# Optimization experiments

Hardware: AMD Instinct MI355X
Metric: run time of the kernel (lower is better)

## Reference

```python
import jax, jax.numpy as jnp
import numpy as np

B, C, H, W = 16, 1024, 64, 64
CH = C // 2
LN_EPS = 1e-5  # F.layer_norm default eps

def setup_inputs() -> dict:
    key = jax.random.key(0)
    ks = jax.random.split(key, 5)
    x = jax.random.normal(ks[0], (B, C, H, W), dtype=jnp.float32)
    # 1x1 conv weights, shape (out_ch, in_ch)
    w_qr = jax.random.normal(ks[1], (1, C), dtype=jnp.float32) * 0.02
    w_vr = jax.random.normal(ks[2], (CH, C), dtype=jnp.float32) * 0.02
    w_ql = jax.random.normal(ks[3], (CH, C), dtype=jnp.float32) * 0.02
    w_vl = jax.random.normal(ks[4], (CH, C), dtype=jnp.float32) * 0.02
    return {"x": x, "w_qr": w_qr, "w_vr": w_vr, "w_ql": w_ql, "w_vl": w_vl}

def reference(x, w_qr, w_vr, w_ql, w_vl):
    b, c, h, w = x.shape
    ch, hw = c // 2, h * w
    # mmcv ConvModule: 1x1 conv (no bias, no norm) + default ReLU activation
    conv = lambda wt: jax.nn.relu(jnp.einsum('bchw,oc->bohw', x, wt))

    # --- spatial attention branch ---
    input_x = conv(w_vr).reshape(b, ch, hw)                       # (b, ch, hw)
    mask = jax.nn.softmax(conv(w_qr).reshape(b, hw), axis=1)      # (b, hw)
    context = jnp.einsum('bcn,bn->bc', input_x, mask)             # (b, ch)
    # layer_norm over (ch,1,1) -> normalize over channel dim, no affine
    mu = jnp.mean(context, axis=1, keepdims=True)
    var = jnp.mean((context - mu) ** 2, axis=1, keepdims=True)
    spatial_attn = jax.nn.sigmoid((context - mu) * jax.lax.rsqrt(var + LN_EPS))[:, :, None]  # (b, ch, 1)

    # --- channel attention branch ---
    g_x = conv(w_ql)                                              # (b, ch, h, w)
    avg_x = jax.nn.softmax(jnp.mean(g_x, axis=(2, 3)), axis=1)    # (b, ch)
    theta_x = conv(w_vl).reshape(b, ch, hw)                       # (b, ch, hw)
    channel_attn = jax.nn.sigmoid(jnp.einsum('bc,bcn->bn', avg_x, theta_x))[:, None, :]  # (b, 1, hw)

    # --- combine ---
    sequence = (spatial_attn * channel_attn).reshape(b, ch, h, w)  # outer product (b, ch, hw)
    parallel = (channel_attn + spatial_attn).reshape(b, ch, h, w)  # broadcast sum
    sk_attn = jnp.concatenate([sequence, parallel], axis=1)        # (b, c, h, w)
    return x * sk_attn + x
```

## Files before the change

### kernel.cpp

```cpp
#include <hip/hip_runtime.h>
#include <cstdint>
#include <cstddef>

#define BATCH 16
#define CIN   1024
#define CH    512
#define HW    4096

static constexpr float LN_EPS = 1e-5f;

typedef __bf16 bf16x8 __attribute__((ext_vector_type(8)));
typedef float  f32x4  __attribute__((ext_vector_type(4)));

__device__ __forceinline__ float sigmoidf_(float v) { return 1.0f / (1.0f + __expf(-v)); }

__device__ __forceinline__ unsigned short f2bf(float f) {
    union { float f; uint32_t u; } c; c.f = f;
    uint32_t r = (c.u + 0x7fffu + ((c.u >> 16) & 1u)) >> 16;
    return (unsigned short)r;
}

#define GLOAD_LDS16(g, l)                                                  \
    __builtin_amdgcn_global_load_lds(                                      \
        (const __attribute__((address_space(1))) void*)(g),                \
        (__attribute__((address_space(3))) void*)(l), 16, 0, 0)

__global__ __launch_bounds__(256) void prep_k(
    const float* __restrict__ x, const float* __restrict__ wqr,
    const float* __restrict__ wvr, const float* __restrict__ wql,
    const float* __restrict__ wvl,
    unsigned short* __restrict__ xt, float* __restrict__ maskpre,
    unsigned short* __restrict__ wA, unsigned short* __restrict__ wB)
{
    __shared__ float t[64][65];
    const int tid = threadIdx.x;
    if (blockIdx.x >= 16384) {
        const int j = (blockIdx.x - 16384) * 256 + tid;
        if (j < 1024 * 1024) {
            const int row = j >> 10, col = j & 1023;
            const float v = (row < 512) ? wql[row * 1024 + col]
                                        : wvr[(row - 512) * 1024 + col];
            wA[j] = f2bf(v);
        } else {
            const int k = j - 1024 * 1024;
            wB[k] = f2bf(wvl[k]);
        }
        return;
    }
    const int nb = blockIdx.x & 63;
    const int cb = (blockIdx.x >> 6) & 15;
    const int b  = blockIdx.x >> 10;
    const int c0 = cb * 64;
    const int n0 = nb * 64;
    const int tx = tid & 15, ty = tid >> 4;
    const float* xb = x + ((size_t)b * CIN + c0) * HW + n0;
#pragma unroll
    for (int rr = 0; rr < 4; ++rr) {
        const int row = ty + rr * 16;
        float4 v = *(const float4*)(xb + (size_t)row * HW + tx * 4);
        t[row][tx * 4 + 0] = v.x; t[row][tx * 4 + 1] = v.y;
        t[row][tx * 4 + 2] = v.z; t[row][tx * 4 + 3] = v.w;
    }
    __syncthreads();
    const int n  = tid >> 2;
    const int cp = (tid & 3) * 16;
    __align__(16) unsigned short tmp[16];
    float part = 0.f;
#pragma unroll
    for (int i = 0; i < 16; ++i) {
        const float v = t[cp + i][n];
        tmp[i] = f2bf(v);
        part = fmaf(wqr[c0 + cp + i], v, part);
    }
    unsigned short* dst = xt + ((size_t)b * HW + n0 + n) * CIN + c0 + cp;
    ((uint4*)dst)[0] = ((const uint4*)tmp)[0];
    ((uint4*)dst)[1] = ((const uint4*)tmp)[1];
    part += __shfl_xor(part, 1);
    part += __shfl_xor(part, 2);
    if ((tid & 3) == 0) atomicAdd(&maskpre[(size_t)b * HW + n0 + n], part);
}

__global__ __launch_bounds__(512) void mfma_gemm256(
    const unsigned short* __restrict__ xt,
    const unsigned short* __restrict__ wst,
    const int MT, const int phase,
    const float* __restrict__ maskp,
    const float* __restrict__ avgx,
    float* __restrict__ gmean,
    float* __restrict__ ctx,
    float* __restrict__ cattnp)
{
    const int nwg = gridDim.x;
    const int per = nwg >> 3;
    const int bid = blockIdx.x;
    const int nid = (bid & 7) * per + (bid >> 3);
    const int mt = nid % MT;
    const int r2 = nid / MT;
    const int nb = r2 & 15;
    const int b  = r2 >> 4;
    const int o0 = mt * 256;
    const int n0 = nb * 256;

    const int tid  = threadIdx.x;
    const int w    = tid >> 6;
    const int lane = tid & 63;
    const int wm = w >> 2;
    const int wn = w & 3;
    const int lr = lane & 15;
    const int hi = lane >> 4;
    const int lr7 = lane & 7;

    __shared__ __align__(16) unsigned short lds[2 * 2 * 2 * 8192];

    f32x4 acc[8][4];
#pragma unroll
    for (int mi = 0; mi < 8; ++mi)
#pragma unroll
        for (int nj = 0; nj < 4; ++nj) acc[mi][nj] = (f32x4){0.f, 0.f, 0.f, 0.f};

    const int sr  = lane >> 3;
    const int ssl = (lane & 7) ^ sr;
    const unsigned short* gA[2][2];
    const unsigned short* gB[2][2];
#pragma unroll
    for (int h = 0; h < 2; ++h)
#pragma unroll
        for (int j = 0; j < 2; ++j) {
            const int row = (w * 2 + j) * 8 + sr;
            gA[h][j] = wst + (size_t)(o0 + h * 128 + row) * CIN + ssl * 8;
            gB[h][j] = xt + ((size_t)b * HW + n0 + h * 128 + row) * CIN + ssl * 8;
        }

#define STG(m, h, tt) do {                                                  \
        unsigned short* lb_ = lds + ((((tt) & 1) * 4) + (m) * 2 + (h)) * 8192 \
                              + (w * 2) * 512;                              \
        const unsigned short* s0_ = ((m) ? gB[h][0] : gA[h][0]) + (tt) * 64; \
        const unsigned short* s1_ = ((m) ? gB[h][1] : gA[h][1]) + (tt) * 64; \
        GLOAD_LDS16(s0_, lb_);                                              \
        GLOAD_LDS16(s1_, lb_ + 512);                                        \
    } while (0)

    const int aoff = lr * 64;
    const int boff = (wn & 1) * 4096 + lr * 64;
    const int sl0 = ((0 + hi) ^ lr7) * 8;
    const int sl1 = ((4 + hi) ^ lr7) * 8;

    bf16x8 bf[4][2];

#define PHASE_BODY(q, c, STAGE_STMT, GATE_STMT) do {                        \
        const unsigned short* Ab_ = lds + ((c) * 4 + wm) * 8192;            \
        const unsigned short* Bb_ = lds + ((c) * 4 + 2 + (wn >> 1)) * 8192; \
        if ((q) == 0) {                                                     \
            _Pragma("unroll")                                               \
            for (int nj = 0; nj < 4; ++nj) {                                \
                bf[nj][0] = *(const bf16x8*)(Bb_ + boff + nj * 1024 + sl0); \
                bf[nj][1] = *(const bf16x8*)(Bb_ + boff + nj * 1024 + sl1); \
            }                                                               \
        }                                                                   \
        bf16x8 af_[2][2];                                                   \
        _Pragma("unroll")                                                   \
        for (int mi = 0; mi < 2; ++mi) {                                    \
            af_[mi][0] = *(const bf16x8*)(Ab_ + ((q) * 32 + mi * 16) * 64 + aoff + sl0); \
            af_[mi][1] = *(const bf16x8*)(Ab_ + ((q) * 32 + mi * 16) * 64 + aoff + sl1); \
        }                                                                   \
        STAGE_STMT;                                                         \
        GATE_STMT;                                                          \
        asm volatile("s_barrier" ::: "memory");                             \
        __builtin_amdgcn_s_setprio(1);                                      \
        _Pragma("unroll")                                                   \
        for (int mi = 0; mi < 2; ++mi)                                      \
            _Pragma("unroll")                                               \
            for (int nj = 0; nj < 4; ++nj) {                                \
                acc[(q) * 2 + mi][nj] = __builtin_amdgcn_mfma_f32_16x16x32_bf16( \
                    af_[mi][0], bf[nj][0], acc[(q) * 2 + mi][nj], 0, 0, 0); \
                acc[(q) * 2 + mi][nj] = __builtin_amdgcn_mfma_f32_16x16x32_bf16( \
                    af_[mi][1], bf[nj][1], acc[(q) * 2 + mi][nj], 0, 0, 0); \
            }                                                               \
        __builtin_amdgcn_s_setprio(0);                                      \
        __builtin_amdgcn_sched_barrier(0);                                  \
        asm volatile("s_barrier" ::: "memory");                             \
    } while (0)

    STG(0, 0, 0); STG(0, 1, 0); STG(1, 0, 0); STG(1, 1, 0);
    STG(1, 0, 1); STG(1, 1, 1); STG(0, 0, 1);
    asm volatile("s_waitcnt vmcnt(6)" ::: "memory");
    asm volatile("s_barrier" ::: "memory");

#pragma unroll 2
    for (int kt = 0; kt < 16; ++kt) {
        const int c = kt & 1;
        PHASE_BODY(0, c, { if (kt < 15) STG(0, 1, kt + 1); }, {});
        PHASE_BODY(1, c, { if (kt < 14) STG(1, 0, kt + 2); }, {});
        PHASE_BODY(2, c, { if (kt < 14) STG(1, 1, kt + 2); }, {});
        PHASE_BODY(3, c, { if (kt < 14) STG(0, 0, kt + 2); },
                   { if (kt < 14)       asm volatile("s_waitcnt vmcnt(6)" ::: "memory");
                     else if (kt == 14) asm volatile("s_waitcnt vmcnt(0)" ::: "memory"); });
    }
#undef PHASE_BODY
#undef STG

    const int quad = hi;
    if (phase == 0) {
        if (mt < 2) {
#pragma unroll
            for (int mr = 0; mr < 8; ++mr)
#pragma unroll
                for (int r = 0; r < 4; ++r) {
                    float v = 0.f;
#pragma unroll
                    for (int nj = 0; nj < 4; ++nj) v += fmaxf(acc[mr][nj][r], 0.f);
                    v += __shfl_xor(v, 1); v += __shfl_xor(v, 2);
                    v += __shfl_xor(v, 4); v += __shfl_xor(v, 8);
                    if (lr == 0)
                        atomicAdd(&gmean[b * CH + o0 + wm * 128 + mr * 16 + quad * 4 + r], v);
                }
        } else {
            float ew[4];
#pragma unroll
            for (int nj = 0; nj < 4; ++nj)
                ew[nj] = __expf(fmaxf(maskp[(size_t)b * HW + n0 + wn * 64 + nj * 16 + lr], 0.f));
#pragma unroll
            for (int mr = 0; mr < 8; ++mr)
#pragma unroll
                for (int r = 0; r < 4; ++r) {
                    float v = 0.f;
#pragma unroll
                    for (int nj = 0; nj < 4; ++nj)
                        v += fmaxf(acc[mr][nj][r], 0.f) * ew[nj];
                    v += __shfl_xor(v, 1); v += __shfl_xor(v, 2);
                    v += __shfl_xor(v, 4); v += __shfl_xor(v, 8);
                    if (lr == 0)
                        atomicAdd(&ctx[b * CH + (o0 - 512) + wm * 128 + mr * 16 + quad * 4 + r], v);
                }
        }
    } else {
        float colsum[4] = {0.f, 0.f, 0.f, 0.f};
#pragma unroll
        for (int mr = 0; mr < 8; ++mr) {
            float aw[4];
#pragma unroll
            for (int r = 0; r < 4; ++r)
                aw[r] = avgx[b * CH + o0 + wm * 128 + mr * 16 + quad * 4 + r];
#pragma unroll
            for (int nj = 0; nj < 4; ++nj)
#pragma unroll
                for (int r = 0; r < 4; ++r)
                    colsum[nj] += fmaxf(acc[mr][nj][r], 0.f) * aw[r];
        }
#pragma unroll
        for (int nj = 0; nj < 4; ++nj) {
            float v = colsum[nj];
            v += __shfl_xor(v, 16);
            v += __shfl_xor(v, 32);
            if (lane < 16)
                atomicAdd(&cattnp[(size_t)b * HW + n0 + wn * 64 + nj * 16 + lane], v);
        }
    }
}

__global__ __launch_bounds__(256) void smch_S_k(const float* __restrict__ gmean,
                                                const float* __restrict__ maskp,
                                                float* __restrict__ avgx,
                                                float* __restrict__ sden)
{
    __shared__ float red[256];
    const int tid = threadIdx.x;
    if (blockIdx.x < 16) {
        const int b = blockIdx.x;
        const float* src = gmean + b * CH;
        float* dst = avgx + b * CH;
        const float v0 = src[tid]       * (1.f / HW);
        const float v1 = src[tid + 256] * (1.f / HW);
        red[tid] = fmaxf(v0, v1); __syncthreads();
        for (int s = 128; s > 0; s >>= 1) { if (tid < s) red[tid] = fmaxf(red[tid], red[tid + s]); __syncthreads(); }
        const float mx = red[0]; __syncthreads();
        const float e0 = __expf(v0 - mx), e1 = __expf(v1 - mx);
        red[tid] = e0 + e1; __syncthreads();
        for (int s = 128; s > 0; s >>= 1) { if (tid < s) red[tid] += red[tid + s]; __syncthreads(); }
        const float inv = 1.f / red[0];
        dst[tid] = e0 * inv; dst[tid + 256] = e1 * inv;
    } else {
        const int b = blockIdx.x - 16;
        const float* row = maskp + (size_t)b * HW;
        float s = 0.f;
        for (int i = tid; i < HW; i += 256) s += __expf(fmaxf(row[i], 0.f));
        red[tid] = s; __syncthreads();
        for (int st = 128; st > 0; st >>= 1) { if (tid < st) red[tid] += red[tid + st]; __syncthreads(); }
        if (tid == 0) sden[b] = red[0];
    }
}

__global__ __launch_bounds__(256) void lnsig_k(const float* __restrict__ ctx,
                                               const float* __restrict__ sden,
                                               float* __restrict__ sattn,
                                               float* __restrict__ cattnp)
{
    const int tid = threadIdx.x;
    if (blockIdx.x >= 16) {
        const int i = (blockIdx.x - 16) * 256 + tid;
        cattnp[i] = sigmoidf_(cattnp[i]);
        return;
    }
    const int b = blockIdx.x;
    const float invS = 1.f / sden[b];
    const float* src = ctx + b * CH;
    __shared__ float red[256];
    const float v0 = src[tid] * invS, v1 = src[tid + 256] * invS;
    red[tid] = v0 + v1; __syncthreads();
    for (int s = 128; s > 0; s >>= 1) { if (tid < s) red[tid] += red[tid + s]; __syncthreads(); }
    const float mu = red[0] * (1.f / CH); __syncthreads();
    const float d0 = v0 - mu, d1 = v1 - mu;
    red[tid] = d0 * d0 + d1 * d1; __syncthreads();
    for (int s = 128; s > 0; s >>= 1) { if (tid < s) red[tid] += red[tid + s]; __syncthreads(); }
    const float rs = rsqrtf(red[0] * (1.f / CH) + LN_EPS);
    sattn[b * CH + tid]       = sigmoidf_(d0 * rs);
    sattn[b * CH + tid + 256] = sigmoidf_(d1 * rs);
}

__global__ __launch_bounds__(256) void final_k(const float* __restrict__ x,
                                               const float* __restrict__ sattn,
                                               const float* __restrict__ cattnp,
                                               float* __restrict__ out)
{
    const int c = blockIdx.x;
    const int b = blockIdx.y;
    const float s = sattn[b * CH + (c & (CH - 1))];
    const bool seq = c < CH;
    const float4* xr = (const float4*)(x + ((size_t)b * CIN + c) * HW);
    const float4* cr = (const float4*)(cattnp + (size_t)b * HW);
    float4* orow = (float4*)(out + ((size_t)b * CIN + c) * HW);
    for (int i = threadIdx.x; i < HW / 4; i += 256) {
        const float4 xv = xr[i], cv = cr[i];
        float4 f;
        if (seq) { f.x = s * cv.x; f.y = s * cv.y; f.z = s * cv.z; f.w = s * cv.w; }
        else     { f.x = s + cv.x; f.y = s + cv.y; f.z = s + cv.z; f.w = s + cv.w; }
        float4 o;
        o.x = fmaf(xv.x, f.x, xv.x);
        o.y = fmaf(xv.y, f.y, xv.y);
        o.z = fmaf(xv.z, f.z, xv.z);
        o.w = fmaf(xv.w, f.w, xv.w);
        orow[i] = o;
    }
}

extern "C" void kernel_launch(void* const* d_in, const int* in_sizes, int n_in,
                              void* d_out, int out_size, void* d_ws, size_t ws_size,
                              hipStream_t stream)
{
    const float* x    = (const float*)d_in[0];
    const float* w_qr = (const float*)d_in[1];
    const float* w_vr = (const float*)d_in[2];
    const float* w_ql = (const float*)d_in[3];
    const float* w_vl = (const float*)d_in[4];
    float* out = (float*)d_out;

    unsigned short* xt = (unsigned short*)d_out;
    unsigned short* wA = xt + (size_t)BATCH * HW * CIN;
    unsigned short* wB = wA + 1024 * CIN;

    float* ws     = (float*)d_ws;
    float* maskp  = ws;
    float* gmean  = maskp + BATCH * HW;
    float* ctx    = gmean + BATCH * CH;
    float* cattnp = ctx   + BATCH * CH;
    float* avgx   = cattnp + BATCH * HW;
    float* sattn  = avgx  + BATCH * CH;
    float* sden   = sattn + BATCH * CH;

    hipMemsetAsync(maskp, 0,
                   (size_t)(BATCH * HW * 2 + BATCH * CH * 2) * sizeof(float), stream);

    prep_k<<<22528, 256, 0, stream>>>(x, w_qr, w_vr, w_ql, w_vl, xt, maskp, wA, wB);

    mfma_gemm256<<<1024, 512, 0, stream>>>(
        xt, wA, 4, 0, maskp, nullptr, gmean, ctx, nullptr);
    smch_S_k<<<32, 256, 0, stream>>>(gmean, maskp, avgx, sden);
    mfma_gemm256<<<512, 512, 0, stream>>>(
        xt, wB, 2, 1, nullptr, avgx, nullptr, nullptr, cattnp);
    lnsig_k<<<272, 256, 0, stream>>>(ctx, sden, sattn, cattnp);
    final_k<<<dim3(CIN, BATCH), 256, 0, stream>>>(x, sattn, cattnp, out);
}
```

Baseline: 721.4 us.

## Make GEMM blocks loop over all M tiles with a continuous K pipeline

Each GEMM workgroup now owns one (batch, 256-column N tile) and walks every 256-row M tile in sequence. The load pipeline runs unbroken across M-tile boundaries, and the per-tile epilogue reductions run inside the loop before the accumulators are reset. This drops the grid to 256 blocks, removing pipeline prologue and drain per tile and letting the B tile stay hot in L2 across M tiles. In exchange there is less parallelism: 256 blocks of 512 threads on a 256-CU part is one wave per CU. Epilogue work inside the loop may also stall the prefetch pipeline.

```diff
diff --git a/kernel.cpp b/kernel.cpp
--- a/kernel.cpp
+++ b/kernel.cpp
@@ -90,15 +90,9 @@
     float* __restrict__ ctx,
     float* __restrict__ cattnp)
 {
-    const int nwg = gridDim.x;
-    const int per = nwg >> 3;
     const int bid = blockIdx.x;
-    const int nid = (bid & 7) * per + (bid >> 3);
-    const int mt = nid % MT;
-    const int r2 = nid / MT;
-    const int nb = r2 & 15;
-    const int b  = r2 >> 4;
-    const int o0 = mt * 256;
+    const int nb = bid & 15;
+    const int b  = bid >> 4;
     const int n0 = nb * 256;
 
     const int tid  = threadIdx.x;
@@ -127,15 +121,18 @@
 #pragma unroll
         for (int j = 0; j < 2; ++j) {
             const int row = (w * 2 + j) * 8 + sr;
-            gA[h][j] = wst + (size_t)(o0 + h * 128 + row) * CIN + ssl * 8;
+            gA[h][j] = wst + (size_t)(h * 128 + row) * CIN + ssl * 8;
             gB[h][j] = xt + ((size_t)b * HW + n0 + h * 128 + row) * CIN + ssl * 8;
         }
 
-#define STG(m, h, tt) do {                                                  \
-        unsigned short* lb_ = lds + ((((tt) & 1) * 4) + (m) * 2 + (h)) * 8192 \
+#define STG(m, h, st) do {                                                  \
+        const int ti_ = (st) >> 4, k_ = (st) & 15;                          \
+        unsigned short* lb_ = lds + ((((st) & 1) * 4) + (m) * 2 + (h)) * 8192 \
                               + (w * 2) * 512;                              \
-        const unsigned short* s0_ = ((m) ? gB[h][0] : gA[h][0]) + (tt) * 64; \
-        const unsigned short* s1_ = ((m) ? gB[h][1] : gA[h][1]) + (tt) * 64; \
+        const unsigned short* s0_ = (m) ? (gB[h][0] + k_ * 64)              \
+                                        : (gA[h][0] + ti_ * (256 * CIN) + k_ * 64); \
+        const unsigned short* s1_ = (m) ? (gB[h][1] + k_ * 64)              \
+                                        : (gA[h][1] + ti_ * (256 * CIN) + k_ * 64); \
         GLOAD_LDS16(s0_, lb_);                                              \
         GLOAD_LDS16(s1_, lb_ + 512);                                        \
     } while (0)
@@ -181,81 +178,90 @@
         asm volatile("s_barrier" ::: "memory");                             \
     } while (0)
 
+    const int T = MT * 16;
+
     STG(0, 0, 0); STG(0, 1, 0); STG(1, 0, 0); STG(1, 1, 0);
     STG(1, 0, 1); STG(1, 1, 1); STG(0, 0, 1);
     asm volatile("s_waitcnt vmcnt(6)" ::: "memory");
     asm volatile("s_barrier" ::: "memory");
 
+    const int quad = hi;
 #pragma unroll 2
-    for (int kt = 0; kt < 16; ++kt) {
-        const int c = kt & 1;
-        PHASE_BODY(0, c, { if (kt < 15) STG(0, 1, kt + 1); }, {});
-        PHASE_BODY(1, c, { if (kt < 14) STG(1, 0, kt + 2); }, {});
-        PHASE_BODY(2, c, { if (kt < 14) STG(1, 1, kt + 2); }, {});
-        PHASE_BODY(3, c, { if (kt < 14) STG(0, 0, kt + 2); },
-                   { if (kt < 14)       asm volatile("s_waitcnt vmcnt(6)" ::: "memory");
-                     else if (kt == 14) asm volatile("s_waitcnt vmcnt(0)" ::: "memory"); });
+    for (int step = 0; step < T; ++step) {
+        const int c = step & 1;
+        PHASE_BODY(0, c, { if (step + 1 < T) STG(0, 1, step + 1); }, {});
+        PHASE_BODY(1, c, { if (step + 2 < T) STG(1, 0, step + 2); }, {});
+        PHASE_BODY(2, c, { if (step + 2 < T) STG(1, 1, step + 2); }, {});
+        PHASE_BODY(3, c, { if (step + 2 < T) STG(0, 0, step + 2); },
+                   { if (step + 2 < T)       asm volatile("s_waitcnt vmcnt(6)" ::: "memory");
+                     else if (step + 2 == T) asm volatile("s_waitcnt vmcnt(0)" ::: "memory"); });
+
+        if ((step & 15) == 15) {
+            const int ti = step >> 4;
+            if (phase == 0) {
+                if (ti < 2) {
+#pragma unroll
+                    for (int mr = 0; mr < 8; ++mr)
+#pragma unroll
+                        for (int r = 0; r < 4; ++r) {
+                            float v = 0.f;
+#pragma unroll
+                            for (int nj = 0; nj < 4; ++nj) v += fmaxf(acc[mr][nj][r], 0.f);
+                            v += __shfl_xor(v, 1); v += __shfl_xor(v, 2);
+                            v += __shfl_xor(v, 4); v += __shfl_xor(v, 8);
+                            if (lr == 0)
+                                atomicAdd(&gmean[b * CH + ti * 256 + wm * 128 + mr * 16 + quad * 4 + r], v);
+                        }
+                } else {
+                    float ew[4];
+#pragma unroll
+                    for (int nj = 0; nj < 4; ++nj)
+                        ew[nj] = __expf(fmaxf(maskp[(size_t)b * HW + n0 + wn * 64 + nj * 16 + lr], 0.f));
+#pragma unroll
+                    for (int mr = 0; mr < 8; ++mr)
+#pragma unroll
+                        for (int r = 0; r < 4; ++r) {
+                            float v = 0.f;
+#pragma unroll
+                            for (int nj = 0; nj < 4; ++nj)
+                                v += fmaxf(acc[mr][nj][r], 0.f) * ew[nj];
+                            v += __shfl_xor(v, 1); v += __shfl_xor(v, 2);
+                            v += __shfl_xor(v, 4); v += __shfl_xor(v, 8);
+                            if (lr == 0)
+                                atomicAdd(&ctx[b * CH + (ti - 2) * 256 + wm * 128 + mr * 16 + quad * 4 + r], v);
+                        }
+                }
+            } else {
+                float colsum[4] = {0.f, 0.f, 0.f, 0.f};
+#pragma unroll
+                for (int mr = 0; mr < 8; ++mr) {
+                    float aw[4];
+#pragma unroll
+                    for (int r = 0; r < 4; ++r)
+                        aw[r] = avgx[b * CH + ti * 256 + wm * 128 + mr * 16 + quad * 4 + r];
+#pragma unroll
+                    for (int nj = 0; nj < 4; ++nj)
+#pragma unroll
+                        for (int r = 0; r < 4; ++r)
+                            colsum[nj] += fmaxf(acc[mr][nj][r], 0.f) * aw[r];
+                }
+#pragma unroll
+                for (int nj = 0; nj < 4; ++nj) {
+                    float v = colsum[nj];
+                    v += __shfl_xor(v, 16);
+                    v += __shfl_xor(v, 32);
+                    if (lane < 16)
+                        atomicAdd(&cattnp[(size_t)b * HW + n0 + wn * 64 + nj * 16 + lane], v);
+                }
+            }
+#pragma unroll
+            for (int mi = 0; mi < 8; ++mi)
+#pragma unroll
+                for (int nj = 0; nj < 4; ++nj) acc[mi][nj] = (f32x4){0.f, 0.f, 0.f, 0.f};
+        }
     }
 #undef PHASE_BODY
 #undef STG
-
-    const int quad = hi;
-    if (phase == 0) {
-        if (mt < 2) {
-#pragma unroll
-            for (int mr = 0; mr < 8; ++mr)
-#pragma unroll
-                for (int r = 0; r < 4; ++r) {
-                    float v = 0.f;
-#pragma unroll
-                    for (int nj = 0; nj < 4; ++nj) v += fmaxf(acc[mr][nj][r], 0.f);
-                    v += __shfl_xor(v, 1); v += __shfl_xor(v, 2);
-                    v += __shfl_xor(v, 4); v += __shfl_xor(v, 8);
-                    if (lr == 0)
-                        atomicAdd(&gmean[b * CH + o0 + wm * 128 + mr * 16 + quad * 4 + r], v);
-                }
-        } else {
-            float ew[4];
-#pragma unroll
-            for (int nj = 0; nj < 4; ++nj)
-                ew[nj] = __expf(fmaxf(maskp[(size_t)b * HW + n0 + wn * 64 + nj * 16 + lr], 0.f));
-#pragma unroll
-            for (int mr = 0; mr < 8; ++mr)
-#pragma unroll
-                for (int r = 0; r < 4; ++r) {
-                    float v = 0.f;
-#pragma unroll
-                    for (int nj = 0; nj < 4; ++nj)
-                        v += fmaxf(acc[mr][nj][r], 0.f) * ew[nj];
-                    v += __shfl_xor(v, 1); v += __shfl_xor(v, 2);
-                    v += __shfl_xor(v, 4); v += __shfl_xor(v, 8);
-                    if (lr == 0)
-                        atomicAdd(&ctx[b * CH + (o0 - 512) + wm * 128 + mr * 16 + quad * 4 + r], v);
-                }
-        }
-    } else {
-        float colsum[4] = {0.f, 0.f, 0.f, 0.f};
-#pragma unroll
-        for (int mr = 0; mr < 8; ++mr) {
-            float aw[4];
-#pragma unroll
-            for (int r = 0; r < 4; ++r)
-                aw[r] = avgx[b * CH + o0 + wm * 128 + mr * 16 + quad * 4 + r];
-#pragma unroll
-            for (int nj = 0; nj < 4; ++nj)
-#pragma unroll
-                for (int r = 0; r < 4; ++r)
-                    colsum[nj] += fmaxf(acc[mr][nj][r], 0.f) * aw[r];
-        }
-#pragma unroll
-        for (int nj = 0; nj < 4; ++nj) {
-            float v = colsum[nj];
-            v += __shfl_xor(v, 16);
-            v += __shfl_xor(v, 32);
-            if (lane < 16)
-                atomicAdd(&cattnp[(size_t)b * HW + n0 + wn * 64 + nj * 16 + lane], v);
-        }
-    }
 }
 
 __global__ __launch_bounds__(256) void smch_S_k(const float* __restrict__ gmean,
@@ -372,10 +378,10 @@
 
     prep_k<<<22528, 256, 0, stream>>>(x, w_qr, w_vr, w_ql, w_vl, xt, maskp, wA, wB);
 
-    mfma_gemm256<<<1024, 512, 0, stream>>>(
+    mfma_gemm256<<<256, 512, 0, stream>>>(
         xt, wA, 4, 0, maskp, nullptr, gmean, ctx, nullptr);
     smch_S_k<<<32, 256, 0, stream>>>(gmean, maskp, avgx, sden);
-    mfma_gemm256<<<512, 512, 0, stream>>>(
+    mfma_gemm256<<<256, 512, 0, stream>>>(
         xt, wB, 2, 1, nullptr, avgx, nullptr, nullptr, cattnp);
     lnsig_k<<<272, 256, 0, stream>>>(ctx, sden, sattn, cattnp);
     final_k<<<dim3(CIN, BATCH), 256, 0, stream>>>(x, sattn, cattnp, out);
```

Measured after the change: 734.6 us. About the same (+1.8%).
